# Performance work log

Hardware: AMD Instinct MI355X
Metric: run time of the kernel (lower is better)

Reference implementation:

```python
import jax, jax.numpy as jnp
import numpy as np

N, E, H, IN = 4096, 65536, 256, 16
N_BLOCKS, N_SUB = 3, 2
IE = 2 * H + 2  # edge-mlp input: h[row] ++ h[col] ++ edge_attr(2)
NORM_FACTOR = 100.0


def setup_inputs() -> dict:
    key = jax.random.key(0)
    ks = jax.random.split(key, 24)
    G = N_BLOCKS * N_SUB  # 6 GCLs total

    def p(k, shape, fan_in, gain=1.0):
        return gain * jax.random.normal(k, shape, jnp.float32) / np.sqrt(fan_in)

    return {
        "h": jax.random.normal(ks[0], (N, IN), jnp.float32),
        "x": jax.random.normal(ks[1], (N, 3), jnp.float32),
        "edge_index": jax.random.randint(ks[2], (2, E), 0, N),
        # embedding in/out
        "emb_w": p(ks[3], (IN, H), IN), "emb_b": jnp.zeros((H,), jnp.float32),
        "out_w": p(ks[4], (H, IN), H), "out_b": jnp.zeros((IN,), jnp.float32),
        # GCL edge MLP (stacked over the 6 GCLs)
        "edge_w1": p(ks[5], (G, IE, H), IE), "edge_b1": jnp.zeros((G, H), jnp.float32),
        "edge_w2": p(ks[6], (G, H, H), H), "edge_b2": jnp.zeros((G, H), jnp.float32),
        # GCL node MLP
        "node_w1": p(ks[7], (G, 2 * H, H), 2 * H), "node_b1": jnp.zeros((G, H), jnp.float32),
        "node_w2": p(ks[8], (G, H, H), H), "node_b2": jnp.zeros((G, H), jnp.float32),
        # EquivariantUpdate coord MLP (stacked over 3 blocks); last layer xavier gain=0.001, no bias
        "coord_w1": p(ks[9], (N_BLOCKS, IE, H), IE), "coord_b1": jnp.zeros((N_BLOCKS, H), jnp.float32),
        "coord_w2": p(ks[10], (N_BLOCKS, H, H), H), "coord_b2": jnp.zeros((N_BLOCKS, H), jnp.float32),
        "coord_w3": p(ks[11], (N_BLOCKS, H, 1), H, gain=0.001),
    }


def reference(h, x, edge_index, emb_w, emb_b, out_w, out_b,
              edge_w1, edge_b1, edge_w2, edge_b2,
              node_w1, node_b1, node_w2, node_b2,
              coord_w1, coord_b1, coord_w2, coord_b2, coord_w3):
    row, col = edge_index[0], edge_index[1]
    n_nodes = h.shape[0]

    def seg_sum(data):  # unsorted_segment_sum with 'sum' aggregation / normalization_factor
        return jax.ops.segment_sum(data, row, num_segments=n_nodes) / NORM_FACTOR

    def coord2diff(xc):  # norm_constant = 1
        d = xc[row] - xc[col]                      # [E,3]
        radial = jnp.sum(d * d, axis=1, keepdims=True)  # [E,1]
        cd = d / (jnp.sqrt(radial + 1e-8) + 1.0)
        return radial, cd

    dist0, _ = coord2diff(x)          # EGNN-level distances (from initial coords)
    h = h @ emb_w + emb_b             # node embedding

    gi = 0
    for b in range(N_BLOCKS):
        radial, coord_diff = coord2diff(x)
        ea = jnp.concatenate([radial, dist0], axis=1)   # [E,2] edge_attr
        for _ in range(N_SUB):  # GCL sublayers
            m = jnp.concatenate([h[row], h[col], ea], axis=1)           # [E, 2H+2]
            m = jax.nn.silu(m @ edge_w1[gi] + edge_b1[gi])
            m = jax.nn.silu(m @ edge_w2[gi] + edge_b2[gi])              # [E, H]
            agg = seg_sum(m)                                            # [N, H]
            u = jnp.concatenate([h, agg], axis=1)                       # [N, 2H]
            u = jax.nn.silu(u @ node_w1[gi] + node_b1[gi])
            h = h + u @ node_w2[gi] + node_b2[gi]                       # residual node update
            gi += 1
        # EquivariantUpdate (tanh=False)
        t = jnp.concatenate([h[row], h[col], ea], axis=1)
        t = jax.nn.silu(t @ coord_w1[b] + coord_b1[b])
        t = jax.nn.silu(t @ coord_w2[b] + coord_b2[b])
        trans = coord_diff * (t @ coord_w3[b])                          # [E,3]
        x = x + seg_sum(trans)

    h = h @ out_w + out_b
    return h, x
```

## Files before the change

kernel.cpp:

```cpp
#include <hip/hip_runtime.h>
#include <hip/hip_bf16.h>
#include <cstdint>
#include <cstddef>

#define NN 4096
#define NE 65536
#define HD 256

typedef __attribute__((ext_vector_type(4))) float f32x4;
typedef __attribute__((ext_vector_type(8))) __bf16 bf16x8;

static __device__ __forceinline__ float silu_f(float v) {
  return v / (1.f + __expf(-v));
}

struct TJob { const float* src; __bf16* dst; int K; int N; };
struct TJobs { TJob j[39]; };

__global__ __launch_bounds__(256) void k_transpose(TJobs jobs) {
  TJob jb = jobs.j[blockIdx.z];
  int k0 = blockIdx.x << 5, n0 = blockIdx.y << 5;
  if (k0 >= jb.K || n0 >= jb.N) return;
  __shared__ float t[32][33];
  int tx = threadIdx.x & 31, ty = threadIdx.x >> 5;
#pragma unroll
  for (int r = ty; r < 32; r += 8)
    t[r][tx] = jb.src[(size_t)(k0 + r) * jb.N + n0 + tx];
  __syncthreads();
#pragma unroll
  for (int r = ty; r < 32; r += 8)
    jb.dst[(size_t)(n0 + r) * jb.K + k0 + tx] = (__bf16)t[tx][r];
}

__global__ __launch_bounds__(256) void k_hist(const int* __restrict__ ei, int* __restrict__ cnt) {
  int e = blockIdx.x * 256 + threadIdx.x;
  atomicAdd(&cnt[ei[e]], 1);
}

__global__ __launch_bounds__(1024) void k_scan(const int* __restrict__ cnt, int* __restrict__ offs,
                                               int* __restrict__ cursor) {
  __shared__ int tmp[1024];
  int tid = threadIdx.x;
  int v[4]; int s = 0;
#pragma unroll
  for (int i = 0; i < 4; i++) { v[i] = cnt[tid * 4 + i]; s += v[i]; }
  tmp[tid] = s;
  __syncthreads();
  for (int o = 1; o < 1024; o <<= 1) {
    int t = (tid >= o) ? tmp[tid - o] : 0;
    __syncthreads();
    tmp[tid] += t;
    __syncthreads();
  }
  int base = (tid > 0) ? tmp[tid - 1] : 0;
#pragma unroll
  for (int i = 0; i < 4; i++) {
    offs[tid * 4 + i] = base; cursor[tid * 4 + i] = base; base += v[i];
  }
  if (tid == 1023) offs[4096] = base;
}

__global__ __launch_bounds__(256) void k_scatter(const int* __restrict__ ei, int* __restrict__ cursor,
                                                 int* __restrict__ elist) {
  int e = blockIdx.x * 256 + threadIdx.x;
  int pos = atomicAdd(&cursor[ei[e]], 1);
  elist[pos] = e;
}

__global__ __launch_bounds__(256) void k_csrinit(const int* __restrict__ elist, const int* __restrict__ ei,
                                                 const float* __restrict__ x, int* __restrict__ rowp,
                                                 int* __restrict__ colp, float* __restrict__ d0p,
                                                 float* __restrict__ xc) {
  int i = blockIdx.x * 256 + threadIdx.x;
  if (i < NN * 3) xc[i] = x[i];
  int e = elist[i];
  int r = ei[e], c = ei[NE + e];
  rowp[i] = r; colp[i] = c;
  float dx = x[r * 3 + 0] - x[c * 3 + 0];
  float dy = x[r * 3 + 1] - x[c * 3 + 1];
  float dz = x[r * 3 + 2] - x[c * 3 + 2];
  d0p[i] = dx * dx + dy * dy + dz * dz;
}

__global__ __launch_bounds__(256) void k_geo(const int* __restrict__ rowp, const int* __restrict__ colp,
                                             const float* __restrict__ x, float* __restrict__ radp,
                                             float* __restrict__ cdp) {
  int i = blockIdx.x * 256 + threadIdx.x;
  int r = rowp[i], c = colp[i];
  float dx = x[r * 3 + 0] - x[c * 3 + 0];
  float dy = x[r * 3 + 1] - x[c * 3 + 1];
  float dz = x[r * 3 + 2] - x[c * 3 + 2];
  float rad = dx * dx + dy * dy + dz * dz;
  radp[i] = rad;
  float inv = 1.f / (sqrtf(rad + 1e-8f) + 1.f);
  cdp[i * 3 + 0] = dx * inv; cdp[i * 3 + 1] = dy * inv; cdp[i * 3 + 2] = dz * inv;
}

__global__ __launch_bounds__(256) void k_embed(const float* __restrict__ h0, const float* __restrict__ W,
                                               const float* __restrict__ b, float* __restrict__ hf,
                                               __bf16* __restrict__ h16) {
  int n = blockIdx.x, c = threadIdx.x;
  float s = b[c];
#pragma unroll
  for (int i = 0; i < 16; i++) s += h0[n * 16 + i] * W[i * 256 + c];
  hf[(size_t)n * HD + c] = s;
  h16[(size_t)n * HD + c] = (__bf16)s;
}

__global__ __launch_bounds__(256) void k_segsum(const __bf16* __restrict__ m2p, const int* __restrict__ offs,
                                                __bf16* __restrict__ agg16) {
  __shared__ float sd[8][256];
  int n = blockIdx.x, t = threadIdx.x;
  int g = t >> 5, l = t & 31;
  int c0 = l << 3;
  float a[8] = {};
  int ib = offs[n], ie = offs[n + 1];
  for (int i = ib + g; i < ie; i += 8) {
    bf16x8 v = *(const bf16x8*)(m2p + (size_t)i * 256 + c0);
#pragma unroll
    for (int j = 0; j < 8; j++) a[j] += (float)v[j];
  }
#pragma unroll
  for (int j = 0; j < 8; j++) sd[g][c0 + j] = a[j];
  __syncthreads();
  float s = 0.f;
#pragma unroll
  for (int j = 0; j < 8; j++) s += sd[j][t];
  agg16[(size_t)n * 256 + t] = (__bf16)(s * 0.01f);
}

__global__ __launch_bounds__(256) void k_xupd(const float* __restrict__ transp, const int* __restrict__ offs,
                                              float* __restrict__ xc) {
  int n = blockIdx.x * 256 + threadIdx.x;
  if (n >= NN) return;
  float a0 = 0.f, a1 = 0.f, a2 = 0.f;
  int i1 = offs[n + 1];
  for (int i = offs[n]; i < i1; i++) {
    a0 += transp[i * 3 + 0]; a1 += transp[i * 3 + 1]; a2 += transp[i * 3 + 2];
  }
  xc[n * 3 + 0] += a0 * 0.01f;
  xc[n * 3 + 1] += a1 * 0.01f;
  xc[n * 3 + 2] += a2 * 0.01f;
}

__global__ __launch_bounds__(256) void k_out(const float* __restrict__ hf, const float* __restrict__ W,
                                             const float* __restrict__ b, const float* __restrict__ xc,
                                             float* __restrict__ out) {
  int t = blockIdx.x * 256 + threadIdx.x;
  if (blockIdx.x < 256) {
    int n = t >> 4, j = t & 15;
    float s = b[j];
    for (int c = 0; c < 256; c++) s += hf[(size_t)n * HD + c] * W[c * 16 + j];
    out[n * 16 + j] = s;
  } else {
    int i = t - NN * 16;
    if (i < NN * 3) out[NN * 16 + i] = xc[i];
  }
}

template <int EPI>
__global__ __launch_bounds__(256, 4) void k_edgeblk(
    const __bf16* __restrict__ PQ, const int* __restrict__ rowp, const int* __restrict__ colp,
    const float* __restrict__ radp, const float* __restrict__ d0p,
    const float* __restrict__ w1r, const float* __restrict__ w1d, const float* __restrict__ b1,
    const __bf16* __restrict__ Bt, const float* __restrict__ b2,
    __bf16* __restrict__ m2p,
    const float* __restrict__ w3, const float* __restrict__ cdp, float* __restrict__ transp) {
  __shared__ alignas(16) char smem[37888];
  float*  wgt = (float*)smem;
  __bf16* Bs0 = (__bf16*)(smem + 5120);
  __bf16* Bs1 = (__bf16*)(smem + 5120 + 16384);
  float*  reds = (float*)(smem + 5120);

  const int tid = threadIdx.x;
  const int lane = tid & 63;
  const int w = tid >> 6;
  const int l15 = lane & 15;
  const int kg = lane >> 4;
  const int R0 = blockIdx.x * 64;
  const int rowg = R0 + w * 16 + l15;

  const __bf16* pBase = PQ + (size_t)rowp[rowg] * 512;
  const __bf16* qBase = PQ + (size_t)colp[rowg] * 512 + 256;
  const float rad = radp[rowg], dd0 = d0p[rowg];

  wgt[tid]       = w1r[tid];
  wgt[256 + tid] = w1d[tid];
  wgt[512 + tid] = b1[tid];
  wgt[768 + tid] = b2[tid];
  if (EPI == 1) wgt[1024 + tid] = w3[tid];

  int srcOff[4], ldsOff[4];
#pragma unroll
  for (int q = 0; q < 4; q++) {
    int s = q * 256 + tid;
    int n = s >> 2, g = s & 3;
    srcOff[q] = n * 256 + ((g ^ ((n >> 1) & 3)) << 3);
    ldsOff[q] = s * 8;
  }

  uint4 rb[4];
#pragma unroll
  for (int q = 0; q < 4; q++) rb[q] = *(const uint4*)(Bt + srcOff[q]);
  bf16x8 pvc = *(const bf16x8*)(pBase + kg * 8);
  bf16x8 qvc = *(const bf16x8*)(qBase + kg * 8);
#pragma unroll
  for (int q = 0; q < 4; q++) *(uint4*)&Bs0[ldsOff[q]] = rb[q];
  __syncthreads();

  f32x4 acc[16] = {};

#pragma unroll
  for (int t = 0; t < 8; t++) {
    const __bf16* Bcur = (t & 1) ? Bs1 : Bs0;
    __bf16*       Bnxt = (t & 1) ? Bs0 : Bs1;
    bf16x8 pvn, qvn;
    if (t < 7) {
      int kt = (t + 1) * 32;
#pragma unroll
      for (int q = 0; q < 4; q++) rb[q] = *(const uint4*)(Bt + kt + srcOff[q]);
      pvn = *(const bf16x8*)(pBase + kt + kg * 8);
      qvn = *(const bf16x8*)(qBase + kt + kg * 8);
    }
    const int k0 = t * 32 + kg * 8;
    f32x4 wr0 = *(const f32x4*)&wgt[k0],       wr1 = *(const f32x4*)&wgt[k0 + 4];
    f32x4 wd0 = *(const f32x4*)&wgt[256 + k0], wd1 = *(const f32x4*)&wgt[256 + k0 + 4];
    f32x4 bb0 = *(const f32x4*)&wgt[512 + k0], bb1 = *(const f32x4*)&wgt[512 + k0 + 4];
    bf16x8 af;
#pragma unroll
    for (int j = 0; j < 4; j++)
      af[j] = (__bf16)silu_f((float)pvc[j] + (float)qvc[j] + rad * wr0[j] + dd0 * wd0[j] + bb0[j]);
#pragma unroll
    for (int j = 0; j < 4; j++)
      af[4 + j] = (__bf16)silu_f((float)pvc[4 + j] + (float)qvc[4 + j] + rad * wr1[j] + dd0 * wd1[j] + bb1[j]);
#pragma unroll
    for (int fn = 0; fn < 16; fn++) {
      int n = fn * 16 + l15;
      bf16x8 bf = *(const bf16x8*)&Bcur[n * 32 + ((kg ^ ((n >> 1) & 3)) << 3)];
      acc[fn] = __builtin_amdgcn_mfma_f32_16x16x32_bf16(af, bf, acc[fn], 0, 0, 0);
    }
    if (t < 7) {
#pragma unroll
      for (int q = 0; q < 4; q++) *(uint4*)&Bnxt[ldsOff[q]] = rb[q];
      pvc = pvn; qvc = qvn;
    }
    __syncthreads();
  }

  if (EPI == 0) {
    __bf16* ep = (__bf16*)(smem + 5120 + w * 4224);
#pragma unroll
    for (int p = 0; p < 2; p++) {
      if ((kg >> 1) == p) {
        int rl = (kg & 1) * 4;
#pragma unroll
        for (int fn = 0; fn < 16; fn++) {
          int col = fn * 16 + l15;
          float bv = wgt[768 + col];
#pragma unroll
          for (int j = 0; j < 4; j++)
            ep[(rl + j) * 264 + col] = (__bf16)silu_f(acc[fn][j] + bv);
        }
      }
      __syncthreads();
#pragma unroll
      for (int i = 0; i < 4; i++) {
        int r = i * 2 + (lane >> 5);
        int g = lane & 31;
        uint4 v = *(const uint4*)&ep[r * 264 + g * 8];
        *(uint4*)(m2p + ((size_t)(R0 + w * 16 + p * 8 + r)) * 256 + g * 8) = v;
      }
      __syncthreads();
    }
  } else {
    float s[4] = {0.f, 0.f, 0.f, 0.f};
#pragma unroll
    for (int fn = 0; fn < 16; fn++) {
      int col = fn * 16 + l15;
      float bv = wgt[768 + col], wv = wgt[1024 + col];
#pragma unroll
      for (int j = 0; j < 4; j++)
        s[j] += silu_f(acc[fn][j] + bv) * wv;
    }
#pragma unroll
    for (int off = 1; off < 16; off <<= 1)
#pragma unroll
      for (int j = 0; j < 4; j++)
        s[j] += __shfl_xor(s[j], off, 64);
    __syncthreads();
    if (l15 == 0) {
#pragma unroll
      for (int j = 0; j < 4; j++)
        reds[w * 16 + kg * 4 + j] = s[j];
    }
    __syncthreads();
    if (tid < 64) {
      float sv = reds[tid];
      size_t i = (size_t)R0 + tid;
      transp[i * 3 + 0] = cdp[i * 3 + 0] * sv;
      transp[i * 3 + 1] = cdp[i * 3 + 1] * sv;
      transp[i * 3 + 2] = cdp[i * 3 + 2] * sv;
    }
  }
}

template <int EPI, int SPLIT>
__global__ __launch_bounds__(256) void k_gemm64(const __bf16* __restrict__ A, const __bf16* __restrict__ A2,
                                                const __bf16* __restrict__ Bt,
                                                const float* __restrict__ bias, __bf16* __restrict__ outb,
                                                float* __restrict__ outf, int M, int N, int K) {
  constexpr int BM = 64, BN = 64, BK = 64;
  __shared__ __bf16 As[2][BM * BK];
  __shared__ __bf16 Bs[2][BN * BK];
  const int tid = threadIdx.x;
  const int lane = tid & 63;
  const int wave = tid >> 6;
  const int wm = wave >> 1, wn = wave & 1;
  const size_t m0 = (size_t)blockIdx.x * BM;
  const size_t n0 = (size_t)blockIdx.y * BN;
  const int r0 = tid >> 3, g0 = tid & 7;
  const int gs0 = (g0 ^ (r0 & 7)) << 3;
  const int Astride = SPLIT ? 256 : K;

  f32x4 acc[2][2] = {};
  const int NT = K >> 6;

  {
    uint4 a0 = *(const uint4*)(A + (m0 + r0) * Astride + g0 * 8);
    uint4 a1 = *(const uint4*)(A + (m0 + r0 + 32) * Astride + g0 * 8);
    uint4 b0 = *(const uint4*)(Bt + (n0 + r0) * K + g0 * 8);
    uint4 b1 = *(const uint4*)(Bt + (n0 + r0 + 32) * K + g0 * 8);
    *(uint4*)&As[0][r0 * BK + gs0] = a0;
    *(uint4*)&As[0][(r0 + 32) * BK + gs0] = a1;
    *(uint4*)&Bs[0][r0 * BK + gs0] = b0;
    *(uint4*)&Bs[0][(r0 + 32) * BK + gs0] = b1;
  }
  __syncthreads();

  int buf = 0;
  for (int t = 0; t < NT; ++t) {
    const bool has = (t + 1 < NT);
    uint4 a0, a1, b0, b1;
    if (has) {
      int kt = (t + 1) << 6;
      const __bf16* Ab;
      int ko;
      if (SPLIT) { Ab = (kt < 256) ? A : A2; ko = kt & 255; }
      else       { Ab = A; ko = kt; }
      a0 = *(const uint4*)(Ab + (m0 + r0) * Astride + ko + g0 * 8);
      a1 = *(const uint4*)(Ab + (m0 + r0 + 32) * Astride + ko + g0 * 8);
      b0 = *(const uint4*)(Bt + (n0 + r0) * K + kt + g0 * 8);
      b1 = *(const uint4*)(Bt + (n0 + r0 + 32) * K + kt + g0 * 8);
    }
#pragma unroll
    for (int ks = 0; ks < BK; ks += 32) {
      const int kg = (ks >> 3) + (lane >> 4);
      bf16x8 af[2], bfv[2];
#pragma unroll
      for (int fm = 0; fm < 2; fm++) {
        int r = wm * 32 + fm * 16 + (lane & 15);
        af[fm] = *(const bf16x8*)&As[buf][r * BK + ((kg ^ (r & 7)) << 3)];
      }
#pragma unroll
      for (int fn = 0; fn < 2; fn++) {
        int r = wn * 32 + fn * 16 + (lane & 15);
        bfv[fn] = *(const bf16x8*)&Bs[buf][r * BK + ((kg ^ (r & 7)) << 3)];
      }
#pragma unroll
      for (int fm = 0; fm < 2; fm++)
#pragma unroll
        for (int fn = 0; fn < 2; fn++)
          acc[fm][fn] = __builtin_amdgcn_mfma_f32_16x16x32_bf16(af[fm], bfv[fn], acc[fm][fn], 0, 0, 0);
    }
    if (has) {
      *(uint4*)&As[buf ^ 1][r0 * BK + gs0] = a0;
      *(uint4*)&As[buf ^ 1][(r0 + 32) * BK + gs0] = a1;
      *(uint4*)&Bs[buf ^ 1][r0 * BK + gs0] = b0;
      *(uint4*)&Bs[buf ^ 1][(r0 + 32) * BK + gs0] = b1;
    }
    __syncthreads();
    buf ^= 1;
  }

#pragma unroll
  for (int fm = 0; fm < 2; fm++) {
#pragma unroll
    for (int fn = 0; fn < 2; fn++) {
      const size_t col = n0 + wn * 32 + fn * 16 + (lane & 15);
      float bv = (EPI == 4) ? 0.f : bias[col];
#pragma unroll
      for (int j = 0; j < 4; j++) {
        size_t row = m0 + wm * 32 + fm * 16 + ((lane >> 4) << 2) + j;
        size_t idx = row * (size_t)N + col;
        float v = acc[fm][fn][j] + bv;
        if (EPI == 1) {
          outb[idx] = (__bf16)silu_f(v);
        } else if (EPI == 2) {
          float nh = outf[idx] + v;
          outf[idx] = nh;
          outb[idx] = (__bf16)nh;
        } else {
          outb[idx] = (__bf16)v;
        }
      }
    }
  }
}

extern "C" void kernel_launch(void* const* d_in, const int* in_sizes, int n_in,
                              void* d_out, int out_size, void* d_ws, size_t ws_size,
                              hipStream_t stream) {
  const float* h_in    = (const float*)d_in[0];
  const float* x_in    = (const float*)d_in[1];
  const int*   ei      = (const int*)d_in[2];
  const float* emb_w   = (const float*)d_in[3];
  const float* emb_b   = (const float*)d_in[4];
  const float* out_w   = (const float*)d_in[5];
  const float* out_b   = (const float*)d_in[6];
  const float* edge_w1 = (const float*)d_in[7];
  const float* edge_b1 = (const float*)d_in[8];
  const float* edge_w2 = (const float*)d_in[9];
  const float* edge_b2 = (const float*)d_in[10];
  const float* node_w1 = (const float*)d_in[11];
  const float* node_b1 = (const float*)d_in[12];
  const float* node_w2 = (const float*)d_in[13];
  const float* node_b2 = (const float*)d_in[14];
  const float* coord_w1 = (const float*)d_in[15];
  const float* coord_b1 = (const float*)d_in[16];
  const float* coord_w2 = (const float*)d_in[17];
  const float* coord_b2 = (const float*)d_in[18];
  const float* coord_w3 = (const float*)d_in[19];

  char* p = (char*)d_ws;
  auto alloc = [&](size_t bytes) -> void* {
    void* r = (void*)p;
    p += (bytes + 255) & ~(size_t)255;
    return r;
  };
  __bf16* e1T  = (__bf16*)alloc((size_t)6 * 512 * 256 * 2);
  __bf16* e2T  = (__bf16*)alloc((size_t)6 * 256 * 256 * 2);
  __bf16* n1T  = (__bf16*)alloc((size_t)6 * 256 * 512 * 2);
  __bf16* n2T  = (__bf16*)alloc((size_t)6 * 256 * 256 * 2);
  __bf16* c1T  = (__bf16*)alloc((size_t)3 * 512 * 256 * 2);
  __bf16* c2T  = (__bf16*)alloc((size_t)3 * 256 * 256 * 2);
  __bf16* h16  = (__bf16*)alloc((size_t)NN * HD * 2);
  __bf16* PQ16 = (__bf16*)alloc((size_t)NN * 512 * 2);
  __bf16* m2p  = (__bf16*)alloc((size_t)NE * HD * 2);
  __bf16* agg16 = (__bf16*)alloc((size_t)NN * HD * 2);
  __bf16* u    = (__bf16*)alloc((size_t)NN * HD * 2);
  float* hf    = (float*)alloc((size_t)NN * HD * 4);
  float* xc    = (float*)alloc((size_t)NN * 3 * 4);
  float* d0p   = (float*)alloc((size_t)NE * 4);
  float* radp  = (float*)alloc((size_t)NE * 4);
  float* cdp   = (float*)alloc((size_t)NE * 3 * 4);
  float* transp = (float*)alloc((size_t)NE * 3 * 4);
  int* cnt     = (int*)alloc((size_t)NN * 4);
  int* offs    = (int*)alloc((size_t)(NN + 1) * 4);
  int* cursor  = (int*)alloc((size_t)NN * 4);
  int* elist   = (int*)alloc((size_t)NE * 4);
  int* rowp    = (int*)alloc((size_t)NE * 4);
  int* colp    = (int*)alloc((size_t)NE * 4);

  TJobs jobs;
  int nj = 0;
  for (int gi = 0; gi < 6; gi++) {
    jobs.j[nj++] = { edge_w1 + (size_t)gi * 514 * 256,             e1T + (size_t)gi * 512 * 256,             256, 256 };
    jobs.j[nj++] = { edge_w1 + (size_t)gi * 514 * 256 + 256 * 256, e1T + (size_t)gi * 512 * 256 + 256 * 256, 256, 256 };
    jobs.j[nj++] = { edge_w2 + (size_t)gi * 256 * 256,             e2T + (size_t)gi * 256 * 256,             256, 256 };
    jobs.j[nj++] = { node_w1 + (size_t)gi * 512 * 256,             n1T + (size_t)gi * 256 * 512,             512, 256 };
    jobs.j[nj++] = { node_w2 + (size_t)gi * 256 * 256,             n2T + (size_t)gi * 256 * 256,             256, 256 };
  }
  for (int b = 0; b < 3; b++) {
    jobs.j[nj++] = { coord_w1 + (size_t)b * 514 * 256,             c1T + (size_t)b * 512 * 256,              256, 256 };
    jobs.j[nj++] = { coord_w1 + (size_t)b * 514 * 256 + 256 * 256, c1T + (size_t)b * 512 * 256 + 256 * 256,  256, 256 };
    jobs.j[nj++] = { coord_w2 + (size_t)b * 256 * 256,             c2T + (size_t)b * 256 * 256,              256, 256 };
  }

  hipMemsetAsync(cnt, 0, (size_t)NN * 4, stream);
  k_transpose<<<dim3(16, 8, 39), 256, 0, stream>>>(jobs);
  k_hist<<<NE / 256, 256, 0, stream>>>(ei, cnt);
  k_scan<<<1, 1024, 0, stream>>>(cnt, offs, cursor);
  k_scatter<<<NE / 256, 256, 0, stream>>>(ei, cursor, elist);
  k_csrinit<<<NE / 256, 256, 0, stream>>>(elist, ei, x_in, rowp, colp, d0p, xc);
  k_embed<<<NN, 256, 0, stream>>>(h_in, emb_w, emb_b, hf, h16);

  int gi = 0;
  for (int b = 0; b < 3; b++) {
    k_geo<<<NE / 256, 256, 0, stream>>>(rowp, colp, xc, radp, cdp);
    for (int s = 0; s < 2; s++, gi++) {
      const float* w1 = edge_w1 + (size_t)gi * 514 * 256;
      k_gemm64<4, 0><<<dim3(64, 8), 256, 0, stream>>>(
          h16, nullptr, e1T + (size_t)gi * 512 * 256, nullptr, PQ16, nullptr, NN, 512, 256);
      k_edgeblk<0><<<NE / 64, 256, 0, stream>>>(
          PQ16, rowp, colp, radp, d0p, w1 + 512 * 256, w1 + 513 * 256, edge_b1 + gi * 256,
          e2T + (size_t)gi * 256 * 256, edge_b2 + gi * 256, m2p, nullptr, nullptr, nullptr);
      k_segsum<<<NN, 256, 0, stream>>>(m2p, offs, agg16);
      k_gemm64<1, 1><<<dim3(64, 4), 256, 0, stream>>>(
          h16, agg16, n1T + (size_t)gi * 256 * 512, node_b1 + gi * 256, u, nullptr, NN, 256, 512);
      k_gemm64<2, 0><<<dim3(64, 4), 256, 0, stream>>>(
          u, nullptr, n2T + (size_t)gi * 256 * 256, node_b2 + gi * 256, h16, hf, NN, 256, 256);
    }
    const float* w1c = coord_w1 + (size_t)b * 514 * 256;
    k_gemm64<4, 0><<<dim3(64, 8), 256, 0, stream>>>(
        h16, nullptr, c1T + (size_t)b * 512 * 256, nullptr, PQ16, nullptr, NN, 512, 256);
    k_edgeblk<1><<<NE / 64, 256, 0, stream>>>(
        PQ16, rowp, colp, radp, d0p, w1c + 512 * 256, w1c + 513 * 256, coord_b1 + b * 256,
        c2T + (size_t)b * 256 * 256, coord_b2 + b * 256, nullptr,
        coord_w3 + (size_t)b * 256, cdp, transp);
    k_xupd<<<NN / 256, 256, 0, stream>>>(transp, offs, xc);
  }
  k_out<<<256 + 48, 256, 0, stream>>>(hf, out_w, out_b, xc, (float*)d_out);
}
```

Measured before the change: 551.5 us.

## Switch edge-block kernel to 32x32x16 MFMA with 128-edge tiles

After: 799.7 us. 1.45x slower.

```diff
diff --git a/kernel.cpp b/kernel.cpp
--- a/kernel.cpp
+++ b/kernel.cpp
@@ -8,6 +8,7 @@
 #define HD 256
 
 typedef __attribute__((ext_vector_type(4))) float f32x4;
+typedef __attribute__((ext_vector_type(16))) float f32x16;
 typedef __attribute__((ext_vector_type(8))) __bf16 bf16x8;
 
 static __device__ __forceinline__ float silu_f(float v) {
@@ -159,7 +160,7 @@
 }
 
 template <int EPI>
-__global__ __launch_bounds__(256, 4) void k_edgeblk(
+__global__ __launch_bounds__(256, 2) void k_edgeblk(
     const __bf16* __restrict__ PQ, const int* __restrict__ rowp, const int* __restrict__ colp,
     const float* __restrict__ radp, const float* __restrict__ d0p,
     const float* __restrict__ w1r, const float* __restrict__ w1d, const float* __restrict__ b1,
@@ -170,19 +171,18 @@
   float*  wgt = (float*)smem;
   __bf16* Bs0 = (__bf16*)(smem + 5120);
   __bf16* Bs1 = (__bf16*)(smem + 5120 + 16384);
-  float*  reds = (float*)(smem + 5120);
 
   const int tid = threadIdx.x;
   const int lane = tid & 63;
   const int w = tid >> 6;
-  const int l15 = lane & 15;
-  const int kg = lane >> 4;
-  const int R0 = blockIdx.x * 64;
-  const int rowg = R0 + w * 16 + l15;
-
-  const __bf16* pBase = PQ + (size_t)rowp[rowg] * 512;
-  const __bf16* qBase = PQ + (size_t)colp[rowg] * 512 + 256;
-  const float rad = radp[rowg], dd0 = d0p[rowg];
+  const int l31 = lane & 31;
+  const int kh = lane >> 5;
+  const int R0 = blockIdx.x * 128;
+  const int erow = R0 + w * 32 + l31;
+
+  const __bf16* pB = PQ + (size_t)rowp[erow] * 512 + kh * 8;
+  const __bf16* qB = PQ + (size_t)colp[erow] * 512 + 256 + kh * 8;
+  const float rad = radp[erow], dd0 = d0p[erow];
 
   wgt[tid]       = w1r[tid];
   wgt[256 + tid] = w1d[tid];
@@ -190,116 +190,117 @@
   wgt[768 + tid] = b2[tid];
   if (EPI == 1) wgt[1024 + tid] = w3[tid];
 
-  int srcOff[4], ldsOff[4];
-#pragma unroll
-  for (int q = 0; q < 4; q++) {
-    int s = q * 256 + tid;
-    int n = s >> 2, g = s & 3;
-    srcOff[q] = n * 256 + ((g ^ ((n >> 1) & 3)) << 3);
-    ldsOff[q] = s * 8;
-  }
+  const int sn0 = w * 64 + (lane & 15);
+  const int sg = lane >> 4;
 
   uint4 rb[4];
 #pragma unroll
-  for (int q = 0; q < 4; q++) rb[q] = *(const uint4*)(Bt + srcOff[q]);
-  bf16x8 pvc = *(const bf16x8*)(pBase + kg * 8);
-  bf16x8 qvc = *(const bf16x8*)(qBase + kg * 8);
-#pragma unroll
-  for (int q = 0; q < 4; q++) *(uint4*)&Bs0[ldsOff[q]] = rb[q];
+  for (int i = 0; i < 4; i++)
+    rb[i] = *(const uint4*)(Bt + (size_t)(sn0 + 16 * i) * 256 + sg * 8);
+  bf16x8 p0c = *(const bf16x8*)(pB);
+  bf16x8 p1c = *(const bf16x8*)(pB + 16);
+  bf16x8 q0c = *(const bf16x8*)(qB);
+  bf16x8 q1c = *(const bf16x8*)(qB + 16);
+#pragma unroll
+  for (int i = 0; i < 4; i++)
+    *(uint4*)&Bs0[sg * 2048 + (sn0 + 16 * i) * 8] = rb[i];
   __syncthreads();
 
-  f32x4 acc[16] = {};
+  f32x16 acc[8] = {};
 
 #pragma unroll
   for (int t = 0; t < 8; t++) {
-    const __bf16* Bcur = (t & 1) ? Bs1 : Bs0;
-    __bf16*       Bnxt = (t & 1) ? Bs0 : Bs1;
-    bf16x8 pvn, qvn;
+    const __bf16* Bc = (t & 1) ? Bs1 : Bs0;
+    __bf16*       Bn = (t & 1) ? Bs0 : Bs1;
+    bf16x8 p0n, p1n, q0n, q1n;
     if (t < 7) {
       int kt = (t + 1) * 32;
 #pragma unroll
-      for (int q = 0; q < 4; q++) rb[q] = *(const uint4*)(Bt + kt + srcOff[q]);
-      pvn = *(const bf16x8*)(pBase + kt + kg * 8);
-      qvn = *(const bf16x8*)(qBase + kt + kg * 8);
-    }
-    const int k0 = t * 32 + kg * 8;
-    f32x4 wr0 = *(const f32x4*)&wgt[k0],       wr1 = *(const f32x4*)&wgt[k0 + 4];
-    f32x4 wd0 = *(const f32x4*)&wgt[256 + k0], wd1 = *(const f32x4*)&wgt[256 + k0 + 4];
-    f32x4 bb0 = *(const f32x4*)&wgt[512 + k0], bb1 = *(const f32x4*)&wgt[512 + k0 + 4];
-    bf16x8 af;
-#pragma unroll
-    for (int j = 0; j < 4; j++)
-      af[j] = (__bf16)silu_f((float)pvc[j] + (float)qvc[j] + rad * wr0[j] + dd0 * wd0[j] + bb0[j]);
-#pragma unroll
-    for (int j = 0; j < 4; j++)
-      af[4 + j] = (__bf16)silu_f((float)pvc[4 + j] + (float)qvc[4 + j] + rad * wr1[j] + dd0 * wd1[j] + bb1[j]);
-#pragma unroll
-    for (int fn = 0; fn < 16; fn++) {
-      int n = fn * 16 + l15;
-      bf16x8 bf = *(const bf16x8*)&Bcur[n * 32 + ((kg ^ ((n >> 1) & 3)) << 3)];
-      acc[fn] = __builtin_amdgcn_mfma_f32_16x16x32_bf16(af, bf, acc[fn], 0, 0, 0);
+      for (int i = 0; i < 4; i++)
+        rb[i] = *(const uint4*)(Bt + (size_t)(sn0 + 16 * i) * 256 + kt + sg * 8);
+      p0n = *(const bf16x8*)(pB + kt);
+      p1n = *(const bf16x8*)(pB + kt + 16);
+      q0n = *(const bf16x8*)(qB + kt);
+      q1n = *(const bf16x8*)(qB + kt + 16);
+    }
+#pragma unroll
+    for (int s = 0; s < 2; s++) {
+      const int k0 = t * 32 + s * 16 + kh * 8;
+      f32x4 wrA = *(const f32x4*)&wgt[k0],       wrB = *(const f32x4*)&wgt[k0 + 4];
+      f32x4 wdA = *(const f32x4*)&wgt[256 + k0], wdB = *(const f32x4*)&wgt[256 + k0 + 4];
+      f32x4 bbA = *(const f32x4*)&wgt[512 + k0], bbB = *(const f32x4*)&wgt[512 + k0 + 4];
+      bf16x8 pv = s ? p1c : p0c;
+      bf16x8 qv = s ? q1c : q0c;
+      bf16x8 af;
+#pragma unroll
+      for (int j = 0; j < 4; j++)
+        af[j] = (__bf16)silu_f((float)pv[j] + (float)qv[j] + rad * wrA[j] + dd0 * wdA[j] + bbA[j]);
+#pragma unroll
+      for (int j = 0; j < 4; j++)
+        af[4 + j] = (__bf16)silu_f((float)pv[4 + j] + (float)qv[4 + j] + rad * wrB[j] + dd0 * wdB[j] + bbB[j]);
+      const int gb = (s * 2 + kh) * 2048;
+#pragma unroll
+      for (int fn = 0; fn < 8; fn++) {
+        bf16x8 bfv = *(const bf16x8*)&Bc[gb + (fn * 32 + l31) * 8];
+        acc[fn] = __builtin_amdgcn_mfma_f32_32x32x16_bf16(af, bfv, acc[fn], 0, 0, 0);
+      }
     }
     if (t < 7) {
 #pragma unroll
-      for (int q = 0; q < 4; q++) *(uint4*)&Bnxt[ldsOff[q]] = rb[q];
-      pvc = pvn; qvc = qvn;
+      for (int i = 0; i < 4; i++)
+        *(uint4*)&Bn[sg * 2048 + (sn0 + 16 * i) * 8] = rb[i];
+      p0c = p0n; p1c = p1n; q0c = q0n; q1c = q1n;
     }
     __syncthreads();
   }
 
   if (EPI == 0) {
-    __bf16* ep = (__bf16*)(smem + 5120 + w * 4224);
-#pragma unroll
-    for (int p = 0; p < 2; p++) {
-      if ((kg >> 1) == p) {
-        int rl = (kg & 1) * 4;
-#pragma unroll
-        for (int fn = 0; fn < 16; fn++) {
-          int col = fn * 16 + l15;
-          float bv = wgt[768 + col];
-#pragma unroll
-          for (int j = 0; j < 4; j++)
-            ep[(rl + j) * 264 + col] = (__bf16)silu_f(acc[fn][j] + bv);
-        }
+    __bf16* ep = (__bf16*)(smem + 5120) + w * 2112;
+#pragma unroll
+    for (int p = 0; p < 4; p++) {
+#pragma unroll
+      for (int fn = 0; fn < 8; fn++) {
+        int col = fn * 32 + l31;
+        float bv = wgt[768 + col];
+#pragma unroll
+        for (int jj = 0; jj < 4; jj++)
+          ep[(jj + 4 * kh) * 264 + col] = (__bf16)silu_f(acc[fn][p * 4 + jj] + bv);
       }
       __syncthreads();
 #pragma unroll
       for (int i = 0; i < 4; i++) {
-        int r = i * 2 + (lane >> 5);
-        int g = lane & 31;
-        uint4 v = *(const uint4*)&ep[r * 264 + g * 8];
-        *(uint4*)(m2p + ((size_t)(R0 + w * 16 + p * 8 + r)) * 256 + g * 8) = v;
+        int row = i * 2 + kh;
+        uint4 v = *(const uint4*)&ep[row * 264 + l31 * 8];
+        *(uint4*)(m2p + (size_t)(R0 + w * 32 + p * 8 + row) * 256 + l31 * 8) = v;
       }
       __syncthreads();
     }
   } else {
-    float s[4] = {0.f, 0.f, 0.f, 0.f};
-#pragma unroll
-    for (int fn = 0; fn < 16; fn++) {
-      int col = fn * 16 + l15;
+    float s[16];
+#pragma unroll
+    for (int j = 0; j < 16; j++) s[j] = 0.f;
+#pragma unroll
+    for (int fn = 0; fn < 8; fn++) {
+      int col = fn * 32 + l31;
       float bv = wgt[768 + col], wv = wgt[1024 + col];
 #pragma unroll
-      for (int j = 0; j < 4; j++)
+      for (int j = 0; j < 16; j++)
         s[j] += silu_f(acc[fn][j] + bv) * wv;
     }
 #pragma unroll
-    for (int off = 1; off < 16; off <<= 1)
-#pragma unroll
-      for (int j = 0; j < 4; j++)
+    for (int off = 1; off < 32; off <<= 1)
+#pragma unroll
+      for (int j = 0; j < 16; j++)
         s[j] += __shfl_xor(s[j], off, 64);
-    __syncthreads();
-    if (l15 == 0) {
-#pragma unroll
-      for (int j = 0; j < 4; j++)
-        reds[w * 16 + kg * 4 + j] = s[j];
-    }
-    __syncthreads();
-    if (tid < 64) {
-      float sv = reds[tid];
-      size_t i = (size_t)R0 + tid;
-      transp[i * 3 + 0] = cdp[i * 3 + 0] * sv;
-      transp[i * 3 + 1] = cdp[i * 3 + 1] * sv;
-      transp[i * 3 + 2] = cdp[i * 3 + 2] * sv;
+#pragma unroll
+    for (int j = 0; j < 16; j++) {
+      if (l31 == j) {
+        int row = (j & 3) + 8 * (j >> 2) + 4 * kh;
+        size_t i = (size_t)R0 + w * 32 + row;
+        transp[i * 3 + 0] = cdp[i * 3 + 0] * s[j];
+        transp[i * 3 + 1] = cdp[i * 3 + 1] * s[j];
+        transp[i * 3 + 2] = cdp[i * 3 + 2] * s[j];
+      }
     }
   }
 }
@@ -491,7 +492,7 @@
       const float* w1 = edge_w1 + (size_t)gi * 514 * 256;
       k_gemm64<4, 0><<<dim3(64, 8), 256, 0, stream>>>(
           h16, nullptr, e1T + (size_t)gi * 512 * 256, nullptr, PQ16, nullptr, NN, 512, 256);
-      k_edgeblk<0><<<NE / 64, 256, 0, stream>>>(
+      k_edgeblk<0><<<NE / 128, 256, 0, stream>>>(
           PQ16, rowp, colp, radp, d0p, w1 + 512 * 256, w1 + 513 * 256, edge_b1 + gi * 256,
           e2T + (size_t)gi * 256 * 256, edge_b2 + gi * 256, m2p, nullptr, nullptr, nullptr);
       k_segsum<<<NN, 256, 0, stream>>>(m2p, offs, agg16);
@@ -503,7 +504,7 @@
     const float* w1c = coord_w1 + (size_t)b * 514 * 256;
     k_gemm64<4, 0><<<dim3(64, 8), 256, 0, stream>>>(
         h16, nullptr, c1T + (size_t)b * 512 * 256, nullptr, PQ16, nullptr, NN, 512, 256);
-    k_edgeblk<1><<<NE / 64, 256, 0, stream>>>(
+    k_edgeblk<1><<<NE / 128, 256, 0, stream>>>(
         PQ16, rowp, colp, radp, d0p, w1c + 512 * 256, w1c + 513 * 256, coord_b1 + b * 256,
         c2T + (size_t)b * 256 * 256, coord_b2 + b * 256, nullptr,
         coord_w3 + (size_t)b * 256, cdp, transp);
```
